# Kernel tuning notes

Measured on AMD Instinct MI355X. Metric: run time of the kernel, lower is better.

## Reference

```python
import jax, jax.numpy as jnp
import numpy as np


def setup_inputs() -> dict:
    key = jax.random.key(0)
    ks = jax.random.split(key, 6)
    B, U, E, D, P = 8, 1024, 1024, 256, 256
    return {
        "u_enc": jax.random.normal(ks[0], (B, U, D), dtype=jnp.float32),
        "e_enc": jax.random.normal(ks[1], (B, E, D), dtype=jnp.float32),
        "pair_enc": jax.random.normal(ks[2], (B, U, E), dtype=jnp.float32),
        "ue_mask": jax.random.uniform(ks[3], (B, U, E), dtype=jnp.float32),
        "w_kernel": jax.random.normal(ks[4], (D, P), dtype=jnp.float32) / np.sqrt(D).astype(np.float32),
        "w_bias": jnp.zeros((P,), dtype=jnp.float32),
        "bpp_w": jnp.ones((), dtype=jnp.float32),
        "bpp_b": jnp.zeros((), dtype=jnp.float32),
    }


def reference(u_enc, e_enc, pair_enc, ue_mask, w_kernel, w_bias, bpp_w, bpp_b):
    # OuterProductUpdate: shared Dense projection of u and e, then outer product.
    u_p = u_enc @ w_kernel + w_bias            # [B,U,P]
    e_p = e_enc @ w_kernel + w_bias            # [B,E,P]
    op = ue_mask * jnp.einsum('bup,bep->bue', u_p, e_p)  # [B,U,E]
    # Sigmoid gate over pair features.
    mask = ue_mask * jax.nn.sigmoid(bpp_w * pair_enc + bpp_b + op)  # [B,U,E]
    # Original: (mask[...,None] * concat(u_rep, e_rep)).sum(axis=(-2,-3)).
    # Algebraically identical without the UxEx2D intermediate:
    #   concat( sum_{u,e} mask * u_enc[u],  sum_{u,e} mask * e_enc[e] )
    u_part = jnp.einsum('bue,bud->bd', mask, u_enc)  # [B,D]
    e_part = jnp.einsum('bue,bed->bd', mask, e_enc)  # [B,D]
    return jnp.concatenate([u_part, e_part], axis=-1)  # [B,2D]
```

## Files before the change

kernel.cpp:

```cpp
#include <hip/hip_runtime.h>

#define BDIM 8
#define UDIM 1024
#define EDIM 1024
#define DDIM 256
#define PDIM 256

typedef __attribute__((ext_vector_type(8))) short bf16x8;
typedef __attribute__((ext_vector_type(4))) float f32x4;

__device__ __forceinline__ short f2bf(float x) {
    unsigned u = __float_as_uint(x);
    unsigned r = (u + 0x7FFFu + ((u >> 16) & 1u)) >> 16;
    return (short)r;
}

__global__ __launch_bounds__(256) void prep_kernel(
    const float* __restrict__ w, ushort* __restrict__ wT,
    float* __restrict__ sums ,
    float* __restrict__ out, int out_size)
{
    int n = blockIdx.x, k = threadIdx.x;
    wT[(size_t)n * PDIM + k] = (ushort)f2bf(w[(size_t)k * PDIM + n]);
    int g = n * 256 + k;
    if (g < BDIM * UDIM + BDIM * EDIM) sums[g] = 0.f;
    if (g < out_size) out[g] = 0.f;
}

__global__ __launch_bounds__(256) void proj_kernel(
    const float* __restrict__ u_enc, const float* __restrict__ e_enc,
    const ushort* __restrict__ wT, const float* __restrict__ bias,
    ushort* __restrict__ u_p, ushort* __restrict__ e_p)
{
    int row0 = blockIdx.x * 64;
    int col0 = blockIdx.y * 64;
    const float* A; ushort* C;
    if (row0 < BDIM * UDIM) { A = u_enc; C = u_p; }
    else                    { A = e_enc; C = e_p; row0 -= BDIM * UDIM; }

    int tid  = threadIdx.x;
    int wave = tid >> 6, lane = tid & 63;
    int m = lane & 15, quad = lane >> 4;

    const float* aptr = A + (size_t)(row0 + wave * 16 + m) * DDIM + quad * 8;

    f32x4 acc[4] = {};

    #pragma unroll
    for (int k0 = 0; k0 < DDIM; k0 += 32) {
        float4 a0 = *(const float4*)(aptr + k0);
        float4 a1 = *(const float4*)(aptr + k0 + 4);
        bf16x8 af;
        af[0] = f2bf(a0.x); af[1] = f2bf(a0.y); af[2] = f2bf(a0.z); af[3] = f2bf(a0.w);
        af[4] = f2bf(a1.x); af[5] = f2bf(a1.y); af[6] = f2bf(a1.z); af[7] = f2bf(a1.w);
        #pragma unroll
        for (int nt = 0; nt < 4; ++nt) {
            bf16x8 bfr = *(const bf16x8*)(wT + (size_t)(col0 + nt * 16 + m) * DDIM + k0 + quad * 8);
            acc[nt] = __builtin_amdgcn_mfma_f32_16x16x32_bf16(af, bfr, acc[nt], 0, 0, 0);
        }
    }

    #pragma unroll
    for (int nt = 0; nt < 4; ++nt) {
        int col = col0 + nt * 16 + m;
        float bv = bias[col];
        #pragma unroll
        for (int r = 0; r < 4; ++r) {
            int row = row0 + wave * 16 + quad * 4 + r;
            C[(size_t)row * PDIM + col] = (ushort)f2bf(acc[nt][r] + bv);
        }
    }
}

__global__ __launch_bounds__(256) void fused_kernel(
    const ushort* __restrict__ u_p, const ushort* __restrict__ e_p,
    const float* __restrict__ pair_enc, const float* __restrict__ ue_mask,
    const float* __restrict__ bpp_w_p, const float* __restrict__ bpp_b_p,
    float* __restrict__ row_sums, float* __restrict__ col_sums)
{
    __shared__ float colred[4][64];

    int b  = blockIdx.y;
    int iu = blockIdx.x >> 4, ie = blockIdx.x & 15;
    int u0 = iu * 64, e0 = ie * 64;

    int tid  = threadIdx.x;
    int wave = tid >> 6, lane = tid & 63;
    int m = lane & 15, quad = lane >> 4;

    const ushort* Au = u_p + (size_t)b * UDIM * PDIM + (size_t)(u0 + wave * 16 + m) * PDIM + quad * 8;
    const ushort* Be = e_p + (size_t)b * EDIM * PDIM + (size_t)(e0 + m) * PDIM + quad * 8;

    f32x4 acc[4] = {};

    #pragma unroll
    for (int k0 = 0; k0 < PDIM; k0 += 32) {
        bf16x8 af = *(const bf16x8*)(Au + k0);
        #pragma unroll
        for (int nt = 0; nt < 4; ++nt) {
            bf16x8 bfr = *(const bf16x8*)(Be + (size_t)nt * 16 * PDIM + k0);
            acc[nt] = __builtin_amdgcn_mfma_f32_16x16x32_bf16(af, bfr, acc[nt], 0, 0, 0);
        }
    }

    float bw = bpp_w_p[0], bb = bpp_b_p[0];
    const float* pm = pair_enc + (size_t)b * UDIM * EDIM;
    const float* mm = ue_mask  + (size_t)b * UDIM * EDIM;

    float rsum[4] = {0.f, 0.f, 0.f, 0.f};
    float csum[4] = {0.f, 0.f, 0.f, 0.f};
    #pragma unroll
    for (int r = 0; r < 4; ++r) {
        int row = u0 + wave * 16 + quad * 4 + r;
        #pragma unroll
        for (int nt = 0; nt < 4; ++nt) {
            int col = e0 + nt * 16 + m;
            size_t idx = (size_t)row * EDIM + col;
            float mv = mm[idx], pv = pm[idx];
            float arg = bw * pv + bb + mv * acc[nt][r];
            float s = mv / (1.f + __expf(-arg));
            rsum[r]  += s;
            csum[nt] += s;
        }
    }

    #pragma unroll
    for (int r = 0; r < 4; ++r) {
        float v = rsum[r];
        v += __shfl_xor(v, 1); v += __shfl_xor(v, 2);
        v += __shfl_xor(v, 4); v += __shfl_xor(v, 8);
        if (m == 0)
            atomicAdd(&row_sums[(size_t)b * UDIM + u0 + wave * 16 + quad * 4 + r], v);
    }

    #pragma unroll
    for (int nt = 0; nt < 4; ++nt) {
        float v = csum[nt];
        v += __shfl_xor(v, 16); v += __shfl_xor(v, 32);
        if (quad == 0) colred[wave][nt * 16 + m] = v;
    }
    __syncthreads();

    if (tid < 64) {
        float v = colred[0][tid] + colred[1][tid] + colred[2][tid] + colred[3][tid];
        atomicAdd(&col_sums[(size_t)b * EDIM + e0 + tid], v);
    }
}

__global__ __launch_bounds__(256) void finish_kernel(
    const float* __restrict__ u_enc, const float* __restrict__ e_enc,
    const float* __restrict__ row_sums, const float* __restrict__ col_sums,
    float* __restrict__ out)
{
    int b = blockIdx.x;
    int half = blockIdx.y;
    int chunk = blockIdx.z;
    int d = threadIdx.x;

    const float* enc = half ? e_enc : u_enc;
    const float* s   = half ? col_sums : row_sums;

    int base = chunk * 64;
    float acc = 0.f;
    #pragma unroll 4
    for (int u = 0; u < 64; ++u) {
        float sv = s[(size_t)b * UDIM + base + u];
        acc += sv * enc[(size_t)(b * UDIM + base + u) * DDIM + d];
    }
    atomicAdd(&out[(size_t)b * 2 * DDIM + half * DDIM + d], acc);
}

extern "C" void kernel_launch(void* const* d_in, const int* in_sizes, int n_in,
                              void* d_out, int out_size, void* d_ws, size_t ws_size,
                              hipStream_t stream)
{
    const float* u_enc    = (const float*)d_in[0];
    const float* e_enc    = (const float*)d_in[1];
    const float* pair_enc = (const float*)d_in[2];
    const float* ue_mask  = (const float*)d_in[3];
    const float* w_kernel = (const float*)d_in[4];
    const float* w_bias   = (const float*)d_in[5];
    const float* bpp_w    = (const float*)d_in[6];
    const float* bpp_b    = (const float*)d_in[7];
    float* out = (float*)d_out;

    ushort* u_p = (ushort*)d_ws;
    ushort* e_p = u_p + (size_t)BDIM * UDIM * PDIM;
    ushort* wT  = e_p + (size_t)BDIM * EDIM * PDIM;
    float* row_sums = (float*)(wT + (size_t)DDIM * PDIM);
    float* col_sums = row_sums + BDIM * UDIM;

    prep_kernel<<<dim3(256), 256, 0, stream>>>(w_kernel, wT, row_sums, out, out_size);

    proj_kernel<<<dim3(256, 4), 256, 0, stream>>>(u_enc, e_enc, wT, w_bias, u_p, e_p);

    fused_kernel<<<dim3(256, BDIM), 256, 0, stream>>>(u_p, e_p, pair_enc, ue_mask,
                                                      bpp_w, bpp_b, row_sums, col_sums);

    finish_kernel<<<dim3(BDIM, 2, 16), 256, 0, stream>>>(u_enc, e_enc, row_sums, col_sums, out);
}
```

Before: 180.2 us.

## Software-pipeline MFMA loads, batch nontemporal streaming loads, widen finish grid

The projection and fused kernels now prefetch the next k-slice of operands into registers while the current MFMAs run. The fused kernel issues all mask and pair loads up front with nontemporal hints so memory latency overlaps. The finish kernel splits work into 64 chunks of 16 rows with four independent accumulators. This raises memory-level parallelism at the cost of more registers and more atomics in the finish stage.

```diff
diff --git a/kernel.cpp b/kernel.cpp
--- a/kernel.cpp
+++ b/kernel.cpp
@@ -17,8 +17,7 @@
 
 __global__ __launch_bounds__(256) void prep_kernel(
     const float* __restrict__ w, ushort* __restrict__ wT,
-    float* __restrict__ sums ,
-    float* __restrict__ out, int out_size)
+    float* __restrict__ sums, float* __restrict__ out, int out_size)
 {
     int n = blockIdx.x, k = threadIdx.x;
     wT[(size_t)n * PDIM + k] = (ushort)f2bf(w[(size_t)k * PDIM + n]);
@@ -42,21 +41,38 @@
     int wave = tid >> 6, lane = tid & 63;
     int m = lane & 15, quad = lane >> 4;
 
-    const float* aptr = A + (size_t)(row0 + wave * 16 + m) * DDIM + quad * 8;
+    const float*  aptr = A + (size_t)(row0 + wave * 16 + m) * DDIM + quad * 8;
+    const ushort* bptr = wT + (size_t)(col0 + m) * DDIM + quad * 8;
 
     f32x4 acc[4] = {};
 
-    #pragma unroll
-    for (int k0 = 0; k0 < DDIM; k0 += 32) {
-        float4 a0 = *(const float4*)(aptr + k0);
-        float4 a1 = *(const float4*)(aptr + k0 + 4);
+    float4 a0c = *(const float4*)(aptr);
+    float4 a1c = *(const float4*)(aptr + 4);
+    bf16x8 bc[4];
+    #pragma unroll
+    for (int nt = 0; nt < 4; ++nt)
+        bc[nt] = *(const bf16x8*)(bptr + (size_t)nt * 16 * DDIM);
+
+    #pragma unroll
+    for (int k0 = 32; k0 <= DDIM; k0 += 32) {
+        float4 a0n, a1n; bf16x8 bn[4];
+        if (k0 < DDIM) {
+            a0n = *(const float4*)(aptr + k0);
+            a1n = *(const float4*)(aptr + k0 + 4);
+            #pragma unroll
+            for (int nt = 0; nt < 4; ++nt)
+                bn[nt] = *(const bf16x8*)(bptr + (size_t)nt * 16 * DDIM + k0);
+        }
         bf16x8 af;
-        af[0] = f2bf(a0.x); af[1] = f2bf(a0.y); af[2] = f2bf(a0.z); af[3] = f2bf(a0.w);
-        af[4] = f2bf(a1.x); af[5] = f2bf(a1.y); af[6] = f2bf(a1.z); af[7] = f2bf(a1.w);
-        #pragma unroll
-        for (int nt = 0; nt < 4; ++nt) {
-            bf16x8 bfr = *(const bf16x8*)(wT + (size_t)(col0 + nt * 16 + m) * DDIM + k0 + quad * 8);
-            acc[nt] = __builtin_amdgcn_mfma_f32_16x16x32_bf16(af, bfr, acc[nt], 0, 0, 0);
+        af[0] = f2bf(a0c.x); af[1] = f2bf(a0c.y); af[2] = f2bf(a0c.z); af[3] = f2bf(a0c.w);
+        af[4] = f2bf(a1c.x); af[5] = f2bf(a1c.y); af[6] = f2bf(a1c.z); af[7] = f2bf(a1c.w);
+        #pragma unroll
+        for (int nt = 0; nt < 4; ++nt)
+            acc[nt] = __builtin_amdgcn_mfma_f32_16x16x32_bf16(af, bc[nt], acc[nt], 0, 0, 0);
+        if (k0 < DDIM) {
+            a0c = a0n; a1c = a1n;
+            #pragma unroll
+            for (int nt = 0; nt < 4; ++nt) bc[nt] = bn[nt];
         }
     }
 
@@ -93,13 +109,28 @@
 
     f32x4 acc[4] = {};
 
-    #pragma unroll
-    for (int k0 = 0; k0 < PDIM; k0 += 32) {
-        bf16x8 af = *(const bf16x8*)(Au + k0);
-        #pragma unroll
-        for (int nt = 0; nt < 4; ++nt) {
-            bf16x8 bfr = *(const bf16x8*)(Be + (size_t)nt * 16 * PDIM + k0);
-            acc[nt] = __builtin_amdgcn_mfma_f32_16x16x32_bf16(af, bfr, acc[nt], 0, 0, 0);
+    bf16x8 ac = *(const bf16x8*)(Au);
+    bf16x8 bc[4];
+    #pragma unroll
+    for (int nt = 0; nt < 4; ++nt)
+        bc[nt] = *(const bf16x8*)(Be + (size_t)nt * 16 * PDIM);
+
+    #pragma unroll
+    for (int k0 = 32; k0 <= PDIM; k0 += 32) {
+        bf16x8 an, bn[4];
+        if (k0 < PDIM) {
+            an = *(const bf16x8*)(Au + k0);
+            #pragma unroll
+            for (int nt = 0; nt < 4; ++nt)
+                bn[nt] = *(const bf16x8*)(Be + (size_t)nt * 16 * PDIM + k0);
+        }
+        #pragma unroll
+        for (int nt = 0; nt < 4; ++nt)
+            acc[nt] = __builtin_amdgcn_mfma_f32_16x16x32_bf16(ac, bc[nt], acc[nt], 0, 0, 0);
+        if (k0 < PDIM) {
+            ac = an;
+            #pragma unroll
+            for (int nt = 0; nt < 4; ++nt) bc[nt] = bn[nt];
         }
     }
 
@@ -107,18 +138,27 @@
     const float* pm = pair_enc + (size_t)b * UDIM * EDIM;
     const float* mm = ue_mask  + (size_t)b * UDIM * EDIM;
 
+    float mv[16], pv[16];
+    #pragma unroll
+    for (int r = 0; r < 4; ++r) {
+        int row = u0 + wave * 16 + quad * 4 + r;
+        #pragma unroll
+        for (int nt = 0; nt < 4; ++nt) {
+            size_t idx = (size_t)row * EDIM + (e0 + nt * 16 + m);
+            mv[r * 4 + nt] = __builtin_nontemporal_load(&mm[idx]);
+            pv[r * 4 + nt] = __builtin_nontemporal_load(&pm[idx]);
+        }
+    }
+
     float rsum[4] = {0.f, 0.f, 0.f, 0.f};
     float csum[4] = {0.f, 0.f, 0.f, 0.f};
     #pragma unroll
     for (int r = 0; r < 4; ++r) {
-        int row = u0 + wave * 16 + quad * 4 + r;
         #pragma unroll
         for (int nt = 0; nt < 4; ++nt) {
-            int col = e0 + nt * 16 + m;
-            size_t idx = (size_t)row * EDIM + col;
-            float mv = mm[idx], pv = pm[idx];
-            float arg = bw * pv + bb + mv * acc[nt][r];
-            float s = mv / (1.f + __expf(-arg));
+            float mvv = mv[r * 4 + nt], pvv = pv[r * 4 + nt];
+            float arg = bw * pvv + bb + mvv * acc[nt][r];
+            float s = mvv / (1.f + __expf(-arg));
             rsum[r]  += s;
             csum[nt] += s;
         }
@@ -160,14 +200,20 @@
     const float* enc = half ? e_enc : u_enc;
     const float* s   = half ? col_sums : row_sums;
 
-    int base = chunk * 64;
-    float acc = 0.f;
-    #pragma unroll 4
-    for (int u = 0; u < 64; ++u) {
-        float sv = s[(size_t)b * UDIM + base + u];
-        acc += sv * enc[(size_t)(b * UDIM + base + u) * DDIM + d];
-    }
-    atomicAdd(&out[(size_t)b * 2 * DDIM + half * DDIM + d], acc);
+    int base = chunk * 16;
+    float sv[16];
+    #pragma unroll
+    for (int u = 0; u < 16; ++u) sv[u] = s[(size_t)b * UDIM + base + u];
+
+    float a0 = 0.f, a1 = 0.f, a2 = 0.f, a3 = 0.f;
+    #pragma unroll
+    for (int u = 0; u < 16; u += 4) {
+        a0 += sv[u + 0] * enc[(size_t)(b * UDIM + base + u + 0) * DDIM + d];
+        a1 += sv[u + 1] * enc[(size_t)(b * UDIM + base + u + 1) * DDIM + d];
+        a2 += sv[u + 2] * enc[(size_t)(b * UDIM + base + u + 2) * DDIM + d];
+        a3 += sv[u + 3] * enc[(size_t)(b * UDIM + base + u + 3) * DDIM + d];
+    }
+    atomicAdd(&out[(size_t)b * 2 * DDIM + half * DDIM + d], (a0 + a1) + (a2 + a3));
 }
 
 extern "C" void kernel_launch(void* const* d_in, const int* in_sizes, int n_in,
@@ -197,5 +243,5 @@
     fused_kernel<<<dim3(256, BDIM), 256, 0, stream>>>(u_p, e_p, pair_enc, ue_mask,
                                                       bpp_w, bpp_b, row_sums, col_sums);
 
-    finish_kernel<<<dim3(BDIM, 2, 16), 256, 0, stream>>>(u_enc, e_enc, row_sums, col_sums, out);
-}
+    finish_kernel<<<dim3(BDIM, 2, 64), 256, 0, stream>>>(u_enc, e_enc, row_sums, col_sums, out);
+}
```

After: 188.6 us. +4.7%, slower.
